# Optimization experiments

Hardware: AMD Instinct MI355X
Metric: run time of the kernel (lower is better)

The kernel has to match this reference:

```python
import jax, jax.numpy as jnp
import numpy as np

B, T, D = 4, 2048, 1024
H = 16
HD = D // H  # 64

def setup_inputs() -> dict:
    key = jax.random.key(0)
    k1, k2, k3, k4, k5 = jax.random.split(key, 5)
    s = 1.0 / np.sqrt(D)
    return {
        "x": jax.random.normal(k1, (B, T, D), dtype=jnp.float32),
        "Wqkv": jax.random.normal(k2, (D, 3 * D), dtype=jnp.float32) * s,
        "bqkv": jnp.zeros((3 * D,), dtype=jnp.float32),
        "Wproj": jax.random.normal(k3, (D, D), dtype=jnp.float32) * s,
        "bproj": jnp.zeros((D,), dtype=jnp.float32),
    }

def reference(x, Wqkv, bqkv, Wproj, bproj):
    Bq, Tq, C = x.shape
    qkv = x @ Wqkv + bqkv                       # [B,T,3D]
    qkv = qkv.reshape(Bq, Tq, 3, H, HD).transpose(2, 0, 3, 1, 4)  # [3,B,H,T,hd]
    q, k, v = qkv[0], qkv[1], qkv[2]
    scale = 1.0 / np.sqrt(HD)
    att = jnp.einsum("bhqd,bhkd->bhqk", q, k) * scale  # [B,H,T,T]
    causal = jnp.tril(jnp.ones((Tq, Tq), dtype=bool))
    att = jnp.where(causal[None, None], att, -jnp.inf)
    att = jax.nn.softmax(att, axis=-1)
    out = jnp.einsum("bhqk,bhkd->bhqd", att, v)        # [B,H,T,hd]
    out = out.transpose(0, 2, 1, 3).reshape(Bq, Tq, C)
    return out @ Wproj + bproj
```

## Files before the change

### kernel.cpp

```cpp
#include <hip/hip_runtime.h>

typedef float f32x4 __attribute__((ext_vector_type(4)));
typedef __bf16 bf16x8 __attribute__((ext_vector_type(8)));
typedef __bf16 bf16x4 __attribute__((ext_vector_type(4)));

#define B_ 4
#define T_ 2048
#define D_ 1024
#define H_ 16
#define HD_ 64

__device__ __forceinline__ void gload_lds16(const void* g, void* l) {
  __builtin_amdgcn_global_load_lds(
      (const __attribute__((address_space(1))) void*)g,
      (__attribute__((address_space(3))) void*)l, 16, 0, 0);
}

__global__ __launch_bounds__(256) void k_cvt_f32_bf16(
    const float* __restrict__ in, __bf16* __restrict__ out, int n4) {
  int i = blockIdx.x * blockDim.x + threadIdx.x;
  int stride = gridDim.x * blockDim.x;
  for (; i < n4; i += stride) {
    float4 v = reinterpret_cast<const float4*>(in)[i];
    bf16x4 o = { (__bf16)v.x, (__bf16)v.y, (__bf16)v.z, (__bf16)v.w };
    reinterpret_cast<bf16x4*>(out)[i] = o;
  }
}

template <typename Tin>
__global__ __launch_bounds__(256) void k_transpose_bf16(
    const Tin* __restrict__ in, __bf16* __restrict__ out,
    int R, int C, long inb, long outb) {
  __shared__ alignas(16) __bf16 lds[64 * 68];
  const int t = threadIdx.x;
  in  += (long)blockIdx.z * inb;
  out += (long)blockIdx.z * outb;
  const int r0 = blockIdx.y * 64, c0 = blockIdx.x * 64;
#pragma unroll
  for (int i = 0; i < 16; ++i) {
    int e = i * 256 + t, row = e >> 6, col = e & 63;
    lds[row * 68 + col] = (__bf16)(float)in[(long)(r0 + row) * C + c0 + col];
  }
  __syncthreads();
#pragma unroll
  for (int i = 0; i < 16; ++i) {
    int e = i * 256 + t, orow = e >> 6, ocol = e & 63;
    out[(long)(c0 + orow) * R + r0 + ocol] = lds[ocol * 68 + orow];
  }
}

template <int EPI>
__global__ __launch_bounds__(256) void k_gemm_bt(
    const __bf16* __restrict__ A, const __bf16* __restrict__ Bt,
    const float* __restrict__ bias, void* __restrict__ Cout,
    __bf16* __restrict__ vout, int M, int N, int K) {
  __shared__ alignas(16) __bf16 As[2][128 * 32];
  __shared__ alignas(16) __bf16 Bs[2][128 * 32];
  const int t = threadIdx.x;
  const int w = t >> 6, l = t & 63;
  const int g = l >> 4, r16 = l & 15;
  const int wr = w >> 1, wc = w & 1;
  const int m0 = blockIdx.y * 128, n0 = blockIdx.x * 128;

  f32x4 acc[4][4];
#pragma unroll
  for (int i = 0; i < 4; ++i)
#pragma unroll
    for (int j = 0; j < 4; ++j) acc[i][j] = (f32x4){0.f, 0.f, 0.f, 0.f};

  const int arow = t >> 2;
  const int acol = ((t & 3) ^ ((t >> 3) & 3)) * 8;
  const char* Ag = (const char*)(A + (long)(m0 + arow) * K + acol);
  const char* Bg = (const char*)(Bt + (long)(n0 + arow) * K + acol);
  const long rowskip = (long)64 * K * 2;
  const int rdsw = (g ^ ((r16 >> 1) & 3)) * 8;

  auto stage = [&](int buf, long koff) {
    char* AsW = (char*)As[buf] + w * 1024;
    char* BsW = (char*)Bs[buf] + w * 1024;
    gload_lds16(Ag + koff, AsW);
    gload_lds16(Ag + koff + rowskip, AsW + 4096);
    gload_lds16(Bg + koff, BsW);
    gload_lds16(Bg + koff + rowskip, BsW + 4096);
  };

  stage(0, 0);
  __syncthreads();

  for (int kt = 0; kt < K; kt += 32) {
    const int cur = (kt >> 5) & 1;
    if (kt + 32 < K) stage(cur ^ 1, (long)(kt + 32) * 2);
    bf16x8 af[4], bfr[4];
#pragma unroll
    for (int mi = 0; mi < 4; ++mi)
      af[mi] = *reinterpret_cast<const bf16x8*>(
          &As[cur][(wr * 64 + mi * 16 + r16) * 32 + rdsw]);
#pragma unroll
    for (int ni = 0; ni < 4; ++ni)
      bfr[ni] = *reinterpret_cast<const bf16x8*>(
          &Bs[cur][(wc * 64 + ni * 16 + r16) * 32 + rdsw]);
    __builtin_amdgcn_s_setprio(1);
#pragma unroll
    for (int mi = 0; mi < 4; ++mi)
#pragma unroll
      for (int ni = 0; ni < 4; ++ni)
        acc[mi][ni] = __builtin_amdgcn_mfma_f32_16x16x32_bf16(af[mi], bfr[ni], acc[mi][ni], 0, 0, 0);
    __builtin_amdgcn_s_setprio(0);
    __syncthreads();
  }

  if (EPI == 0) {
    const int which = n0 >> 10;
    __bf16* qkvb = (__bf16*)Cout;
#pragma unroll
    for (int mi = 0; mi < 4; ++mi) {
#pragma unroll
      for (int ni = 0; ni < 4; ++ni) {
        const int n = n0 + wc * 64 + ni * 16 + r16;
        const float bv = bias[n];
        f32x4 c = acc[mi][ni];
        const int rem = n & 1023, h = rem >> 6, hd = rem & 63;
        const int mbase = m0 + wr * 64 + mi * 16 + g * 4;
        const int b = mbase >> 11, tt0 = mbase & 2047;
        if (which < 2) {
#pragma unroll
          for (int r = 0; r < 4; ++r)
            qkvb[((long)((which * B_ + b) * H_ + h) * T_ + tt0 + r) * HD_ + hd] =
                (__bf16)(c[r] + bv);
        } else {
          bf16x4 pk = { (__bf16)(c[0] + bv), (__bf16)(c[1] + bv),
                        (__bf16)(c[2] + bv), (__bf16)(c[3] + bv) };
          *reinterpret_cast<bf16x4*>(
              &vout[(((long)b * H_ + h) * HD_ + hd) * T_ + tt0]) = pk;
        }
      }
    }
  } else {
    float* O = (float*)Cout;
#pragma unroll
    for (int mi = 0; mi < 4; ++mi) {
#pragma unroll
      for (int ni = 0; ni < 4; ++ni) {
        const int n = n0 + wc * 64 + ni * 16 + r16;
        const float bv = bias[n];
        f32x4 c = acc[mi][ni];
        const int mbase = m0 + wr * 64 + mi * 16 + g * 4;
#pragma unroll
        for (int r = 0; r < 4; ++r) O[(long)(mbase + r) * N + n] = c[r] + bv;
      }
    }
  }
}

__device__ __forceinline__ void soft_side(
    const f32x4 (&s)[4], float& lrun, bool diag, int qrel,
    int g, int r16, bf16x8& pa0, bf16x8& pa1) {
  float p[4][4];
#pragma unroll
  for (int nf = 0; nf < 4; ++nf) {
#pragma unroll
    for (int rr = 0; rr < 4; ++rr) {
      float x = s[nf][rr];
      if (diag) x = (nf * 16 + 4 * g + rr <= qrel + r16) ? x : -1e30f;
      p[nf][rr] = __builtin_amdgcn_exp2f(x);
    }
  }
  const float ps0 = (p[0][0] + p[0][1]) + (p[0][2] + p[0][3]);
  const float ps1 = (p[1][0] + p[1][1]) + (p[1][2] + p[1][3]);
  const float ps2 = (p[2][0] + p[2][1]) + (p[2][2] + p[2][3]);
  const float ps3 = (p[3][0] + p[3][1]) + (p[3][2] + p[3][3]);
  lrun += (ps0 + ps1) + (ps2 + ps3);

  unsigned u[4][2];
#pragma unroll
  for (int nf = 0; nf < 4; ++nf) {
    asm("v_cvt_pk_bf16_f32 %0, %1, %2"
        : "=v"(u[nf][0]) : "v"(p[nf][0]), "v"(p[nf][1]));
    asm("v_cvt_pk_bf16_f32 %0, %1, %2"
        : "=v"(u[nf][1]) : "v"(p[nf][2]), "v"(p[nf][3]));
  }
#pragma unroll
  for (int j = 0; j < 2; ++j) {
    asm("v_permlane32_swap_b32 %0, %1" : "+v"(u[0][j]), "+v"(u[1][j]));
    asm("v_permlane32_swap_b32 %0, %1" : "+v"(u[2][j]), "+v"(u[3][j]));
  }
#pragma unroll
  for (int j = 0; j < 2; ++j) {
    asm("v_permlane16_swap_b32 %0, %1" : "+v"(u[0][j]), "+v"(u[1][j]));
    asm("v_permlane16_swap_b32 %0, %1" : "+v"(u[2][j]), "+v"(u[3][j]));
  }
  union PU { unsigned w[4]; bf16x8 v; };
  PU a0, a1;
  a0.w[0] = u[0][0]; a0.w[1] = u[0][1]; a0.w[2] = u[1][0]; a0.w[3] = u[1][1];
  a1.w[0] = u[2][0]; a1.w[1] = u[2][1]; a1.w[2] = u[3][0]; a1.w[3] = u[3][1];
  pa0 = a0.v;
  pa1 = a1.v;
}

__global__ __launch_bounds__(256) void k_attn(
    const __bf16* __restrict__ q, const __bf16* __restrict__ k,
    const __bf16* __restrict__ vt, __bf16* __restrict__ o) {
  __shared__ alignas(16) __bf16 Ks[2][64 * 64];
  __shared__ alignas(16) __bf16 Vs[2][64 * 64];
  const int t = threadIdx.x, w = t >> 6, l = t & 63;
  const int g = l >> 4, r16 = l & 15;
  const int bh = blockIdx.x;
  const int qt = 31 - blockIdx.y;
  const int qbase = qt * 64 + w * 16;
  const float sc = 0.125f * 1.44269504088896341f;

  auto scale8 = [&](bf16x8 v) {
    bf16x8 r;
#pragma unroll
    for (int j = 0; j < 8; ++j) r[j] = (__bf16)((float)v[j] * sc);
    return r;
  };
  const __bf16* qp = q + ((long)bh * T_ + qbase + r16) * HD_ + g * 8;
  const bf16x8 aq0 = scale8(*reinterpret_cast<const bf16x8*>(qp));
  const bf16x8 aq1 = scale8(*reinterpret_cast<const bf16x8*>(qp + 32));

  f32x4 oacc[4];
  float lrun = 0.f;
#pragma unroll
  for (int i = 0; i < 4; ++i) oacc[i] = (f32x4){0.f, 0.f, 0.f, 0.f};

  const int srow = t >> 3, sslot = t & 7;
  const int sswz = sslot ^ (srow & 7);
  const char* kg = (const char*)(k + ((long)bh * T_ + srow) * HD_) + sswz * 16;
  const char* vg = (const char*)(vt + ((long)bh * HD_ + srow) * T_) + sswz * 16;

  auto stage = [&](int buf, int kv0) {
    char* Kd = (char*)Ks[buf] + w * 1024;
    char* Vd = (char*)Vs[buf] + w * 1024;
    gload_lds16(kg + (long)kv0 * 128, Kd);
    gload_lds16(kg + (long)kv0 * 128 + 32 * 128, Kd + 4096);
    gload_lds16(vg + (long)kv0 * 2, Vd);
    gload_lds16(vg + (long)kv0 * 2 + 32 * (long)T_ * 2, Vd + 4096);
  };

  stage(0, 0);
  __syncthreads();

  const int ntile = qt + 1;
  for (int it = 0; it < ntile; ++it) {
    const int cur = it & 1;
    if (it + 1 < ntile) stage(cur ^ 1, (it + 1) * 64);
    const char* Kc = (const char*)Ks[cur];
    const char* Vc = (const char*)Vs[cur];

    f32x4 s[4];
    __builtin_amdgcn_s_setprio(1);
#pragma unroll
    for (int nf = 0; nf < 4; ++nf) {
      const char* kb = Kc + (nf * 16 + r16) * 128;
      const bf16x8 b0 = *reinterpret_cast<const bf16x8*>(kb + ((g ^ (r16 & 7)) << 4));
      const bf16x8 b1 = *reinterpret_cast<const bf16x8*>(kb + (((4 + g) ^ (r16 & 7)) << 4));
      f32x4 z = (f32x4){0.f, 0.f, 0.f, 0.f};
      z = __builtin_amdgcn_mfma_f32_16x16x32_bf16(b0, aq0, z, 0, 0, 0);
      z = __builtin_amdgcn_mfma_f32_16x16x32_bf16(b1, aq1, z, 0, 0, 0);
      s[nf] = z;
    }
    __builtin_amdgcn_s_setprio(0);

    bf16x8 pa0, pa1;
    soft_side(s, lrun, it == qt, qbase - it * 64, g, r16, pa0, pa1);

    __builtin_amdgcn_s_setprio(1);
#pragma unroll
    for (int nf = 0; nf < 4; ++nf) {
      const char* vb = Vc + (nf * 16 + r16) * 128;
      const bf16x8 v0 = *reinterpret_cast<const bf16x8*>(vb + ((g ^ (r16 & 7)) << 4));
      const bf16x8 v1 = *reinterpret_cast<const bf16x8*>(vb + (((4 + g) ^ (r16 & 7)) << 4));
      oacc[nf] = __builtin_amdgcn_mfma_f32_16x16x32_bf16(pa0, v0, oacc[nf], 0, 0, 0);
      oacc[nf] = __builtin_amdgcn_mfma_f32_16x16x32_bf16(pa1, v1, oacc[nf], 0, 0, 0);
    }
    __builtin_amdgcn_s_setprio(0);
    __syncthreads();
  }

  lrun += __shfl_xor(lrun, 16, 64);
  lrun += __shfl_xor(lrun, 32, 64);
  const float inv = 1.f / lrun;
  float invq[4];
#pragma unroll
  for (int rr = 0; rr < 4; ++rr) invq[rr] = __shfl(inv, 4 * g + rr, 64);
  const int b = bh >> 4, h = bh & 15;
#pragma unroll
  for (int nf = 0; nf < 4; ++nf) {
    const int hd = nf * 16 + r16;
#pragma unroll
    for (int rr = 0; rr < 4; ++rr) {
      const int tt = qbase + g * 4 + rr;
      o[((long)b * T_ + tt) * D_ + h * HD_ + hd] = (__bf16)(oacc[nf][rr] * invq[rr]);
    }
  }
}

extern "C" void kernel_launch(void* const* d_in, const int* in_sizes, int n_in,
                              void* d_out, int out_size, void* d_ws, size_t ws_size,
                              hipStream_t stream) {
  (void)in_sizes; (void)n_in; (void)out_size; (void)ws_size;
  const float* x     = (const float*)d_in[0];
  const float* Wqkv  = (const float*)d_in[1];
  const float* bqkv  = (const float*)d_in[2];
  const float* Wproj = (const float*)d_in[3];
  const float* bproj = (const float*)d_in[4];
  float* out = (float*)d_out;

  const long MT = (long)B_ * T_;
  __bf16* xb     = (__bf16*)d_ws;
  __bf16* wqkvt  = xb + MT * D_;
  __bf16* wprojt = wqkvt + (long)3 * D_ * D_;
  __bf16* qkvb   = wprojt + (long)D_ * D_;
  __bf16* vtb    = qkvb + (long)2 * B_ * H_ * T_ * HD_;
  __bf16* attno  = vtb + (long)B_ * H_ * HD_ * T_;

  k_cvt_f32_bf16<<<2048, 256, 0, stream>>>(x, xb, (int)(MT * D_ / 4));
  k_transpose_bf16<float><<<dim3(48, 16, 1), 256, 0, stream>>>(Wqkv, wqkvt, D_, 3 * D_, 0, 0);
  k_transpose_bf16<float><<<dim3(16, 16, 1), 256, 0, stream>>>(Wproj, wprojt, D_, D_, 0, 0);
  k_gemm_bt<0><<<dim3(24, 64), 256, 0, stream>>>(xb, wqkvt, bqkv, qkvb, vtb, 8192, 3072, 1024);
  k_attn<<<dim3(64, 32), 256, 0, stream>>>(
      qkvb, qkvb + (long)B_ * H_ * T_ * HD_, vtb, attno);
  k_gemm_bt<1><<<dim3(8, 64), 256, 0, stream>>>(attno, wprojt, bproj, out, nullptr, 8192, 1024, 1024);
}
```

Baseline: 163.8 us.

## Double attention query tile per block to 128 rows, two 16-row groups per wave

Each block of the attention kernel now covers 128 query rows instead of 64, and each wave keeps two 16-row query fragments. Every K/V tile staged in LDS therefore feeds twice as many MFMAs, which halves K/V global traffic and LDS reads per query row. Waves whose rows lie entirely before a KV tile skip its compute. The costs are more registers per wave, half as many blocks in the grid, and more causal imbalance inside a block near the diagonal.

After: 174.1 us. 1.06x slower.

```diff
diff --git a/kernel.cpp b/kernel.cpp
--- a/kernel.cpp
+++ b/kernel.cpp
@@ -205,8 +205,9 @@
   const int t = threadIdx.x, w = t >> 6, l = t & 63;
   const int g = l >> 4, r16 = l & 15;
   const int bh = blockIdx.x;
-  const int qt = 31 - blockIdx.y;
-  const int qbase = qt * 64 + w * 16;
+  const int qt = 15 - blockIdx.y;
+  const int qbaseW = qt * 128 + w * 32;
+  const int gbaseLo = qbaseW, gbaseHi = qbaseW + 16;
   const float sc = 0.125f * 1.44269504088896341f;
 
   auto scale8 = [&](bf16x8 v) {
@@ -215,14 +216,20 @@
     for (int j = 0; j < 8; ++j) r[j] = (__bf16)((float)v[j] * sc);
     return r;
   };
-  const __bf16* qp = q + ((long)bh * T_ + qbase + r16) * HD_ + g * 8;
-  const bf16x8 aq0 = scale8(*reinterpret_cast<const bf16x8*>(qp));
-  const bf16x8 aq1 = scale8(*reinterpret_cast<const bf16x8*>(qp + 32));
-
-  f32x4 oacc[4];
-  float lrun = 0.f;
-#pragma unroll
-  for (int i = 0; i < 4; ++i) oacc[i] = (f32x4){0.f, 0.f, 0.f, 0.f};
+  const __bf16* qpLo = q + ((long)bh * T_ + gbaseLo + r16) * HD_ + g * 8;
+  const bf16x8 aqLo0 = scale8(*reinterpret_cast<const bf16x8*>(qpLo));
+  const bf16x8 aqLo1 = scale8(*reinterpret_cast<const bf16x8*>(qpLo + 32));
+  const __bf16* qpHi = q + ((long)bh * T_ + gbaseHi + r16) * HD_ + g * 8;
+  const bf16x8 aqHi0 = scale8(*reinterpret_cast<const bf16x8*>(qpHi));
+  const bf16x8 aqHi1 = scale8(*reinterpret_cast<const bf16x8*>(qpHi + 32));
+
+  f32x4 oLo[4], oHi[4];
+  float lLo = 0.f, lHi = 0.f;
+#pragma unroll
+  for (int i = 0; i < 4; ++i) {
+    oLo[i] = (f32x4){0.f, 0.f, 0.f, 0.f};
+    oHi[i] = (f32x4){0.f, 0.f, 0.f, 0.f};
+  }
 
   const int srow = t >> 3, sslot = t & 7;
   const int sswz = sslot ^ (srow & 7);
@@ -241,57 +248,78 @@
   stage(0, 0);
   __syncthreads();
 
-  const int ntile = qt + 1;
+  const int ntile = qt * 2 + 2;
   for (int it = 0; it < ntile; ++it) {
     const int cur = it & 1;
     if (it + 1 < ntile) stage(cur ^ 1, (it + 1) * 64);
     const char* Kc = (const char*)Ks[cur];
     const char* Vc = (const char*)Vs[cur];
-
-    f32x4 s[4];
-    __builtin_amdgcn_s_setprio(1);
-#pragma unroll
-    for (int nf = 0; nf < 4; ++nf) {
-      const char* kb = Kc + (nf * 16 + r16) * 128;
-      const bf16x8 b0 = *reinterpret_cast<const bf16x8*>(kb + ((g ^ (r16 & 7)) << 4));
-      const bf16x8 b1 = *reinterpret_cast<const bf16x8*>(kb + (((4 + g) ^ (r16 & 7)) << 4));
-      f32x4 z = (f32x4){0.f, 0.f, 0.f, 0.f};
-      z = __builtin_amdgcn_mfma_f32_16x16x32_bf16(b0, aq0, z, 0, 0, 0);
-      z = __builtin_amdgcn_mfma_f32_16x16x32_bf16(b1, aq1, z, 0, 0, 0);
-      s[nf] = z;
-    }
-    __builtin_amdgcn_s_setprio(0);
-
-    bf16x8 pa0, pa1;
-    soft_side(s, lrun, it == qt, qbase - it * 64, g, r16, pa0, pa1);
-
-    __builtin_amdgcn_s_setprio(1);
-#pragma unroll
-    for (int nf = 0; nf < 4; ++nf) {
-      const char* vb = Vc + (nf * 16 + r16) * 128;
-      const bf16x8 v0 = *reinterpret_cast<const bf16x8*>(vb + ((g ^ (r16 & 7)) << 4));
-      const bf16x8 v1 = *reinterpret_cast<const bf16x8*>(vb + (((4 + g) ^ (r16 & 7)) << 4));
-      oacc[nf] = __builtin_amdgcn_mfma_f32_16x16x32_bf16(pa0, v0, oacc[nf], 0, 0, 0);
-      oacc[nf] = __builtin_amdgcn_mfma_f32_16x16x32_bf16(pa1, v1, oacc[nf], 0, 0, 0);
-    }
-    __builtin_amdgcn_s_setprio(0);
+    const int kv0 = it * 64;
+    const bool live = kv0 <= qbaseW + 31;
+
+    if (live) {
+      const bool diagLo = (kv0 + 63) > gbaseLo;
+      const bool diagHi = (kv0 + 63) > gbaseHi;
+
+      f32x4 sLo[4], sHi[4];
+      __builtin_amdgcn_s_setprio(1);
+#pragma unroll
+      for (int nf = 0; nf < 4; ++nf) {
+        const char* kb = Kc + (nf * 16 + r16) * 128;
+        const bf16x8 b0 = *reinterpret_cast<const bf16x8*>(kb + ((g ^ (r16 & 7)) << 4));
+        const bf16x8 b1 = *reinterpret_cast<const bf16x8*>(kb + (((4 + g) ^ (r16 & 7)) << 4));
+        f32x4 z = (f32x4){0.f, 0.f, 0.f, 0.f};
+        z = __builtin_amdgcn_mfma_f32_16x16x32_bf16(b0, aqLo0, z, 0, 0, 0);
+        z = __builtin_amdgcn_mfma_f32_16x16x32_bf16(b1, aqLo1, z, 0, 0, 0);
+        sLo[nf] = z;
+        f32x4 zh = (f32x4){0.f, 0.f, 0.f, 0.f};
+        zh = __builtin_amdgcn_mfma_f32_16x16x32_bf16(b0, aqHi0, zh, 0, 0, 0);
+        zh = __builtin_amdgcn_mfma_f32_16x16x32_bf16(b1, aqHi1, zh, 0, 0, 0);
+        sHi[nf] = zh;
+      }
+      __builtin_amdgcn_s_setprio(0);
+
+      bf16x8 paLo0, paLo1, paHi0, paHi1;
+      soft_side(sLo, lLo, diagLo, gbaseLo - kv0, g, r16, paLo0, paLo1);
+      soft_side(sHi, lHi, diagHi, gbaseHi - kv0, g, r16, paHi0, paHi1);
+
+      __builtin_amdgcn_s_setprio(1);
+#pragma unroll
+      for (int nf = 0; nf < 4; ++nf) {
+        const char* vb = Vc + (nf * 16 + r16) * 128;
+        const bf16x8 v0 = *reinterpret_cast<const bf16x8*>(vb + ((g ^ (r16 & 7)) << 4));
+        const bf16x8 v1 = *reinterpret_cast<const bf16x8*>(vb + (((4 + g) ^ (r16 & 7)) << 4));
+        oLo[nf] = __builtin_amdgcn_mfma_f32_16x16x32_bf16(paLo0, v0, oLo[nf], 0, 0, 0);
+        oLo[nf] = __builtin_amdgcn_mfma_f32_16x16x32_bf16(paLo1, v1, oLo[nf], 0, 0, 0);
+        oHi[nf] = __builtin_amdgcn_mfma_f32_16x16x32_bf16(paHi0, v0, oHi[nf], 0, 0, 0);
+        oHi[nf] = __builtin_amdgcn_mfma_f32_16x16x32_bf16(paHi1, v1, oHi[nf], 0, 0, 0);
+      }
+      __builtin_amdgcn_s_setprio(0);
+    }
     __syncthreads();
   }
 
-  lrun += __shfl_xor(lrun, 16, 64);
-  lrun += __shfl_xor(lrun, 32, 64);
-  const float inv = 1.f / lrun;
-  float invq[4];
-#pragma unroll
-  for (int rr = 0; rr < 4; ++rr) invq[rr] = __shfl(inv, 4 * g + rr, 64);
+  lLo += __shfl_xor(lLo, 16, 64);
+  lLo += __shfl_xor(lLo, 32, 64);
+  lHi += __shfl_xor(lHi, 16, 64);
+  lHi += __shfl_xor(lHi, 32, 64);
+  const float invLo = 1.f / lLo, invHi = 1.f / lHi;
+  float invLoQ[4], invHiQ[4];
+#pragma unroll
+  for (int rr = 0; rr < 4; ++rr) {
+    invLoQ[rr] = __shfl(invLo, 4 * g + rr, 64);
+    invHiQ[rr] = __shfl(invHi, 4 * g + rr, 64);
+  }
   const int b = bh >> 4, h = bh & 15;
 #pragma unroll
   for (int nf = 0; nf < 4; ++nf) {
     const int hd = nf * 16 + r16;
 #pragma unroll
     for (int rr = 0; rr < 4; ++rr) {
-      const int tt = qbase + g * 4 + rr;
-      o[((long)b * T_ + tt) * D_ + h * HD_ + hd] = (__bf16)(oacc[nf][rr] * invq[rr]);
+      const int ttLo = gbaseLo + g * 4 + rr;
+      o[((long)b * T_ + ttLo) * D_ + h * HD_ + hd] = (__bf16)(oLo[nf][rr] * invLoQ[rr]);
+      const int ttHi = gbaseHi + g * 4 + rr;
+      o[((long)b * T_ + ttHi) * D_ + h * HD_ + hd] = (__bf16)(oHi[nf][rr] * invHiQ[rr]);
     }
   }
 }
@@ -319,7 +347,7 @@
   k_transpose_bf16<float><<<dim3(48, 16, 1), 256, 0, stream>>>(Wqkv, wqkvt, D_, 3 * D_, 0, 0);
   k_transpose_bf16<float><<<dim3(16, 16, 1), 256, 0, stream>>>(Wproj, wprojt, D_, D_, 0, 0);
   k_gemm_bt<0><<<dim3(24, 64), 256, 0, stream>>>(xb, wqkvt, bqkv, qkvb, vtb, 8192, 3072, 1024);
-  k_attn<<<dim3(64, 32), 256, 0, stream>>>(
+  k_attn<<<dim3(64, 16), 256, 0, stream>>>(
       qkvb, qkvb + (long)B_ * H_ * T_ * HD_, vtb, attno);
   k_gemm_bt<1><<<dim3(8, 64), 256, 0, stream>>>(attno, wprojt, bproj, out, nullptr, 8192, 1024, 1024);
 }
```

## Replace QKV GEMM with 256x256-tile 512-thread kernel using swizzled direct-to-LDS loads

Applied to the files above, without the earlier changes.

Adds a dedicated QKV projection GEMM that uses 256x256 output tiles, 8 waves, and a K-step of 64. Operands are loaded straight into LDS with an XOR swizzle, and the next tile is prefetched with split A/B staging inside the MFMA loop, using setprio around the MFMAs. The larger tile raises arithmetic intensity and cuts global traffic compared with the 128x128 kernel. In exchange the grid shrinks to 384 blocks, LDS use and register pressure rise (128 accumulator floats per thread), and occupancy falls.

Measured after the change: 161.4 us. Within noise of the previous version (-1.4%).

```diff
diff --git a/kernel.cpp b/kernel.cpp
--- a/kernel.cpp
+++ b/kernel.cpp
@@ -46,6 +46,108 @@
   for (int i = 0; i < 16; ++i) {
     int e = i * 256 + t, orow = e >> 6, ocol = e & 63;
     out[(long)(c0 + orow) * R + r0 + ocol] = lds[ocol * 68 + orow];
+  }
+}
+
+__global__ __launch_bounds__(512) void k_gemm256_qkv(
+    const __bf16* __restrict__ A, const __bf16* __restrict__ Bt,
+    const float* __restrict__ bias, __bf16* __restrict__ qkvb,
+    __bf16* __restrict__ vout) {
+  __shared__ alignas(16) __bf16 lds[2][2][256 * 64];
+  const int t = threadIdx.x;
+  const int w = t >> 6, l = t & 63;
+  const int g = l >> 4, r16 = l & 15;
+  const int wm = w >> 2, wn = w & 3;
+  const int m0 = blockIdx.y * 256, n0 = blockIdx.x * 256;
+  const int K = 1024, NT = 16;
+
+  f32x4 acc[8][4];
+#pragma unroll
+  for (int i = 0; i < 8; ++i)
+#pragma unroll
+    for (int j = 0; j < 4; ++j) acc[i][j] = (f32x4){0.f, 0.f, 0.f, 0.f};
+
+  auto stageA = [&](int buf, int kt) {
+#pragma unroll
+    for (int c = 0; c < 4; ++c) {
+      const int e = c * 512 + t;
+      const int row = e >> 3, p = e & 7;
+      gload_lds16(A + (long)(m0 + row) * K + kt * 64 + ((p ^ (row & 7)) << 3),
+                  (char*)&lds[buf][0][0] + (c * 512 + w * 64) * 16);
+    }
+  };
+  auto stageB = [&](int buf, int kt) {
+#pragma unroll
+    for (int c = 0; c < 4; ++c) {
+      const int e = c * 512 + t;
+      const int row = e >> 3, p = e & 7;
+      gload_lds16(Bt + (long)(n0 + row) * K + kt * 64 + ((p ^ (row & 7)) << 3),
+                  (char*)&lds[buf][1][0] + (c * 512 + w * 64) * 16);
+    }
+  };
+
+  stageA(0, 0);
+  stageB(0, 0);
+
+  for (int kt = 0; kt < NT; ++kt) {
+    const int cur = kt & 1;
+    const int kn = (kt + 1 < NT) ? kt + 1 : kt;
+    __builtin_amdgcn_s_barrier();
+    stageA(cur ^ 1, kn);
+    asm volatile("s_waitcnt vmcnt(4)" ::: "memory");
+    __builtin_amdgcn_sched_barrier(0);
+    __builtin_amdgcn_s_barrier();
+    const __bf16* Ab = &lds[cur][0][0];
+    const __bf16* Bb = &lds[cur][1][0];
+
+#pragma unroll
+    for (int ks = 0; ks < 2; ++ks) {
+      bf16x8 afr[8], bfr[4];
+      const int slot = ((ks * 4 + g) ^ (r16 & 7)) << 3;
+#pragma unroll
+      for (int mi = 0; mi < 8; ++mi)
+        afr[mi] = *reinterpret_cast<const bf16x8*>(
+            &Ab[(wm * 128 + mi * 16 + r16) * 64 + slot]);
+#pragma unroll
+      for (int ni = 0; ni < 4; ++ni)
+        bfr[ni] = *reinterpret_cast<const bf16x8*>(
+            &Bb[(wn * 64 + ni * 16 + r16) * 64 + slot]);
+      __builtin_amdgcn_s_setprio(1);
+#pragma unroll
+      for (int mi = 0; mi < 8; ++mi)
+#pragma unroll
+        for (int ni = 0; ni < 4; ++ni)
+          acc[mi][ni] = __builtin_amdgcn_mfma_f32_16x16x32_bf16(
+              afr[mi], bfr[ni], acc[mi][ni], 0, 0, 0);
+      __builtin_amdgcn_s_setprio(0);
+      if (ks == 0) stageB(cur ^ 1, kn);
+    }
+  }
+  asm volatile("s_waitcnt vmcnt(0)" ::: "memory");
+
+  const int which = n0 >> 10;
+#pragma unroll
+  for (int mi = 0; mi < 8; ++mi) {
+#pragma unroll
+    for (int ni = 0; ni < 4; ++ni) {
+      const int n = n0 + wn * 64 + ni * 16 + r16;
+      const float bv = bias[n];
+      f32x4 c = acc[mi][ni];
+      const int rem = n & 1023, h = rem >> 6, hd = rem & 63;
+      const int mbase = m0 + wm * 128 + mi * 16 + g * 4;
+      const int b = mbase >> 11, tt0 = mbase & 2047;
+      if (which < 2) {
+#pragma unroll
+        for (int r = 0; r < 4; ++r)
+          qkvb[((long)((which * B_ + b) * H_ + h) * T_ + tt0 + r) * HD_ + hd] =
+              (__bf16)(c[r] + bv);
+      } else {
+        bf16x4 pk = { (__bf16)(c[0] + bv), (__bf16)(c[1] + bv),
+                      (__bf16)(c[2] + bv), (__bf16)(c[3] + bv) };
+        *reinterpret_cast<bf16x4*>(
+            &vout[(((long)b * H_ + h) * HD_ + hd) * T_ + tt0]) = pk;
+      }
+    }
   }
 }
 
@@ -318,7 +420,7 @@
   k_cvt_f32_bf16<<<2048, 256, 0, stream>>>(x, xb, (int)(MT * D_ / 4));
   k_transpose_bf16<float><<<dim3(48, 16, 1), 256, 0, stream>>>(Wqkv, wqkvt, D_, 3 * D_, 0, 0);
   k_transpose_bf16<float><<<dim3(16, 16, 1), 256, 0, stream>>>(Wproj, wprojt, D_, D_, 0, 0);
-  k_gemm_bt<0><<<dim3(24, 64), 256, 0, stream>>>(xb, wqkvt, bqkv, qkvb, vtb, 8192, 3072, 1024);
+  k_gemm256_qkv<<<dim3(12, 32), 512, 0, stream>>>(xb, wqkvt, bqkv, qkvb, vtb);
   k_attn<<<dim3(64, 32), 256, 0, stream>>>(
       qkvb, qkvb + (long)B_ * H_ * T_ * HD_, vtb, attno);
   k_gemm_bt<1><<<dim3(8, 64), 256, 0, stream>>>(attno, wprojt, bproj, out, nullptr, 8192, 1024, 1024);
```
